# Performance work log

Measured on AMD Instinct MI355X. Metric: run time of the kernel, lower is better.

The kernel has to match this reference:

```python
import jax, jax.numpy as jnp
import numpy as np

EPSILON = 0.1
MAX_ITER = 100
THRESHOLD = 0.001
NORMALIZE = True
INPUT_SCALE = 0.02  # keeps exp(-cost/eps) from underflowing with randn inputs


def setup_inputs() -> dict:
    key = jax.random.key(0)
    k1, k2 = jax.random.split(key)
    compressed_tokens = jax.random.normal(k1, (16, 64, 768), dtype=jnp.float32) * INPUT_SCALE
    original_tokens = jax.random.normal(k2, (16, 1024, 768), dtype=jnp.float32) * INPUT_SCALE
    return {"compressed_tokens": compressed_tokens, "original_tokens": original_tokens}


def _cost_matrix(source, target):
    # pairwise squared Euclidean distances: (n, m)
    source_sq = jnp.sum(source ** 2, axis=1, keepdims=True)          # (n, 1)
    target_sq = jnp.sum(target ** 2, axis=1, keepdims=True)          # (m, 1)
    cross = source @ target.T                                         # (n, m)
    return source_sq + target_sq.T - 2.0 * cross


def _sinkhorn(K, a, b):
    n, m = K.shape
    u0 = jnp.ones((n,), K.dtype)
    v0 = jnp.ones((m,), K.dtype)

    def step(carry, _):
        u, v, done = carry
        u_new = a / (K @ v + 1e-10)
        v_new = b / (K.T @ u_new + 1e-10)
        err = jnp.max(jnp.abs(u_new - u))
        # torch breaks AFTER the update, so the converged u,v are post-update;
        # once done, freeze u,v (equivalent to breaking out of the loop)
        u_next = jnp.where(done, u, u_new)
        v_next = jnp.where(done, v, v_new)
        done_next = done | (err < THRESHOLD)
        return (u_next, v_next, done_next), None

    (u, v, _), _ = jax.lax.scan(step, (u0, v0, jnp.asarray(False)), None, length=MAX_ITER)
    return u, v


def reference(compressed_tokens, original_tokens):
    d = compressed_tokens.shape[-1]
    src = compressed_tokens.reshape(-1, d)   # (n, d)
    tgt = original_tokens.reshape(-1, d)     # (m, d)
    n, m = src.shape[0], tgt.shape[0]

    cost = _cost_matrix(src, tgt)            # (n, m)
    K = jnp.exp(-cost / EPSILON)
    a = jnp.full((n,), 1.0 / n, dtype=cost.dtype)
    b = jnp.full((m,), 1.0 / m, dtype=cost.dtype)

    u, v = _sinkhorn(K, a, b)

    # <P, C> with P = diag(u) K diag(v)
    ot_distance = jnp.sum((u[:, None] * K * v[None, :]) * cost)
    if NORMALIZE:
        ot_distance = ot_distance / (n + m)
    ot_loss = jnp.sqrt(ot_distance + 1e-8)
    return ot_loss
```

## Files before the change

kernel.cpp:

```cpp
#include <hip/hip_runtime.h>

#define NSRC 1024
#define MTGT 16384
#define DDIM 768
#define MAXIT 100
#define NBLK 256
#define NTHR 1024
#define NGRP 16
#define GRPSZ 16

typedef __attribute__((ext_vector_type(8))) short bf16x8;
typedef __attribute__((ext_vector_type(4))) float f32x4;
typedef __attribute__((ext_vector_type(4))) unsigned short u16x4;
typedef __attribute__((ext_vector_type(8))) unsigned short u16x8;

__device__ __forceinline__ unsigned short f2bf(float f) {
  unsigned u = __float_as_uint(f);
  u += 0x7FFFu + ((u >> 16) & 1u);
  return (unsigned short)(u >> 16);
}
__device__ __forceinline__ float bf2f(unsigned short h) {
  return __uint_as_float(((unsigned)h) << 16);
}
__device__ __forceinline__ void gstoref(float* p, float x) {
  __hip_atomic_store(p, x, __ATOMIC_RELAXED, __HIP_MEMORY_SCOPE_AGENT);
}
__device__ __forceinline__ float gloadf(const float* p) {
  return __hip_atomic_load(p, __ATOMIC_RELAXED, __HIP_MEMORY_SCOPE_AGENT);
}
__device__ __forceinline__ unsigned gloadu(const unsigned* p) {
  return __hip_atomic_load(p, __ATOMIC_RELAXED, __HIP_MEMORY_SCOPE_AGENT);
}
__device__ __forceinline__ void gl_lds16(const unsigned short* g, unsigned short* l) {
  __builtin_amdgcn_global_load_lds((__attribute__((address_space(1))) void*)g,
                                   (__attribute__((address_space(3))) void*)l, 16, 0, 0);
}

__global__ __launch_bounds__(192) void ot_convert_kernel(
    const float* __restrict__ src, const float* __restrict__ tgt,
    unsigned short* __restrict__ srcb, unsigned short* __restrict__ tgtb,
    float* __restrict__ ssq, float* __restrict__ tsq, unsigned* __restrict__ zreg) {
  __shared__ float sbuf[3];
  const int row = blockIdx.x;
  const float* inp;
  unsigned short* outp;
  if (row < NSRC) { inp = src + (size_t)row * DDIM; outp = srcb + (size_t)row * DDIM; }
  else { inp = tgt + (size_t)(row - NSRC) * DDIM; outp = tgtb + (size_t)(row - NSRC) * DDIM; }
  float4 v = *(const float4*)(inp + threadIdx.x * 4);
  u16x4 b; b[0] = f2bf(v.x); b[1] = f2bf(v.y); b[2] = f2bf(v.z); b[3] = f2bf(v.w);
  *(u16x4*)(outp + threadIdx.x * 4) = b;
  float acc = v.x * v.x + v.y * v.y + v.z * v.z + v.w * v.w;
  #pragma unroll
  for (int off = 32; off > 0; off >>= 1) acc += __shfl_down(acc, off, 64);
  int wave = threadIdx.x >> 6, lane = threadIdx.x & 63;
  if (lane == 0) sbuf[wave] = acc;
  __syncthreads();
  if (threadIdx.x == 0) {
    float t = sbuf[0] + sbuf[1] + sbuf[2];
    if (row < NSRC) ssq[row] = t; else tsq[row - NSRC] = t;
  }
  if (row < 576) zreg[row * 192 + threadIdx.x] = 0u;
}

__global__ __launch_bounds__(256) void ot_gemmk_kernel(
    const unsigned short* __restrict__ srcb, const unsigned short* __restrict__ tgtb,
    const float* __restrict__ ssq, const float* __restrict__ tsq,
    unsigned short* __restrict__ Kb, float* __restrict__ rowsum) {
  __shared__ __align__(16) unsigned short As[128 * 64];
  __shared__ __align__(16) unsigned short Bs[128 * 64];
  const int tile = (blockIdx.x & 7) * 128 + (blockIdx.x >> 3);
  const int tm = tile & 7, tn = tile >> 3;
  const int row0 = tm * 128, col0 = tn * 128;
  const int tid = threadIdx.x, lane = tid & 63, wave = tid >> 6;
  const int wm = wave >> 1, wn = wave & 1;
  const int lr = lane & 15, hi = lane >> 4;

  f32x4 acc[4][4];
  #pragma unroll
  for (int fi = 0; fi < 4; ++fi)
    #pragma unroll
    for (int fj = 0; fj < 4; ++fj) acc[fi][fj] = (f32x4){0.f, 0.f, 0.f, 0.f};

  for (int kt = 0; kt < DDIM / 64; ++kt) {
    __syncthreads();
    #pragma unroll
    for (int q = 0; q < 4; ++q) {
      int ch = tid + q * 256;
      int r = ch >> 3, c = ch & 7;
      int cg = c ^ (r & 7);
      gl_lds16(srcb + (size_t)(row0 + r) * DDIM + kt * 64 + cg * 8, As + ch * 8);
      gl_lds16(tgtb + (size_t)(col0 + r) * DDIM + kt * 64 + cg * 8, Bs + ch * 8);
    }
    __syncthreads();
    #pragma unroll
    for (int kc = 0; kc < 2; ++kc) {
      bf16x8 a[4], b[4];
      #pragma unroll
      for (int f = 0; f < 4; ++f) {
        int ra = wm * 64 + f * 16 + lr;
        a[f] = *(const bf16x8*)(As + ra * 64 + ((((kc << 2) | hi) ^ (ra & 7)) << 3));
        int rb = wn * 64 + f * 16 + lr;
        b[f] = *(const bf16x8*)(Bs + rb * 64 + ((((kc << 2) | hi) ^ (rb & 7)) << 3));
      }
      #pragma unroll
      for (int fi = 0; fi < 4; ++fi)
        #pragma unroll
        for (int fj = 0; fj < 4; ++fj)
          acc[fi][fj] = __builtin_amdgcn_mfma_f32_16x16x32_bf16(a[fi], b[fj], acc[fi][fj], 0, 0, 0);
    }
  }

  const float SC = 14.426950408889634f;
  int colv[4]; float tqv[4];
  #pragma unroll
  for (int fj = 0; fj < 4; ++fj) {
    colv[fj] = col0 + wn * 64 + fj * 16 + lr;
    tqv[fj] = tsq[colv[fj]];
  }
  #pragma unroll
  for (int fi = 0; fi < 4; ++fi) {
    #pragma unroll
    for (int e = 0; e < 4; ++e) {
      int row = row0 + wm * 64 + fi * 16 + hi * 4 + e;
      float sq = ssq[row];
      float p = 0.f;
      #pragma unroll
      for (int fj = 0; fj < 4; ++fj) {
        float cost = sq + tqv[fj] - 2.0f * acc[fi][fj][e];
        float k = exp2f(-SC * cost);
        Kb[(size_t)row * MTGT + colv[fj]] = f2bf(k);
        p += k;
      }
      p += __shfl_xor(p, 1, 64);
      p += __shfl_xor(p, 2, 64);
      p += __shfl_xor(p, 4, 64);
      p += __shfl_xor(p, 8, 64);
      if (lr == 0) atomicAdd(&rowsum[row], p);
    }
  }
}

__device__ __forceinline__ void grid_barrier(unsigned* garr, unsigned* root,
                                             unsigned* gen, unsigned& t) {
  __syncthreads();
  if (threadIdx.x == 0) {
    asm volatile("s_waitcnt vmcnt(0)" ::: "memory");
    unsigned g = (unsigned)(blockIdx.x >> 4);
    unsigned old = __hip_atomic_fetch_add(&garr[g * 64], 1u, __ATOMIC_RELAXED,
                                          __HIP_MEMORY_SCOPE_AGENT);
    if (old == t * GRPSZ + (GRPSZ - 1)) {
      unsigned r = __hip_atomic_fetch_add(root, 1u, __ATOMIC_RELAXED,
                                          __HIP_MEMORY_SCOPE_AGENT);
      if (r == t * NGRP + (NGRP - 1)) {
        __hip_atomic_store(gen, t + 1u, __ATOMIC_RELAXED, __HIP_MEMORY_SCOPE_AGENT);
      } else {
        while (gloadu(gen) < t + 1u) __builtin_amdgcn_s_sleep(1);
      }
    } else {
      while (gloadu(gen) < t + 1u) __builtin_amdgcn_s_sleep(1);
    }
    t += 1u;
  }
  __syncthreads();
}

__global__ __launch_bounds__(NTHR) void ot_sinkhorn_kernel(
    const unsigned short* __restrict__ Kb, const float* __restrict__ rowsum,
    float* Kv, float* ot, float* __restrict__ out,
    unsigned* garr, unsigned* root, unsigned* gen) {
  __shared__ float ulds[NSRC];
  __shared__ float vlds[64];
  __shared__ float red[2048];
  __shared__ int sflag[1];
  const int tid = threadIdx.x, bid = blockIdx.x;
  const int w = tid >> 6, l = tid & 63;
  const int r8 = l >> 3, c8 = l & 7;
  const size_t colbase = (size_t)bid * 64 + c8 * 8;
  unsigned bt = 0;
  const float A_VAL = 1.0f / NSRC, B_VAL = 1.0f / MTGT;
  float uold = 1.0f;

  for (int it = 0; it < MAXIT; ++it) {
    float kv;
    if (it == 0) {
      kv = rowsum[tid];
    } else {
      float4 va = *(const float4*)(&vlds[c8 * 8]);
      float4 vb = *(const float4*)(&vlds[c8 * 8 + 4]);
      float p[8];
      #pragma unroll
      for (int t = 0; t < 8; ++t) {
        int i = t * 128 + w * 8 + r8;
        u16x8 k8 = *(const u16x8*)(Kb + (size_t)i * MTGT + colbase);
        p[t] = bf2f(k8[0]) * va.x + bf2f(k8[1]) * va.y +
               bf2f(k8[2]) * va.z + bf2f(k8[3]) * va.w +
               bf2f(k8[4]) * vb.x + bf2f(k8[5]) * vb.y +
               bf2f(k8[6]) * vb.z + bf2f(k8[7]) * vb.w;
      }
      #pragma unroll
      for (int t = 0; t < 8; ++t) {
        p[t] += __shfl_xor(p[t], 1, 64);
        p[t] += __shfl_xor(p[t], 2, 64);
        p[t] += __shfl_xor(p[t], 4, 64);
      }
      float* kvs = Kv + (size_t)(it - 1) * NSRC;
      if (c8 == 0) {
        #pragma unroll
        for (int t = 0; t < 8; ++t) atomicAdd(&kvs[t * 128 + w * 8 + r8], p[t]);
      }
      grid_barrier(garr, root, gen, bt);
      kv = gloadf(&kvs[tid]);
    }
    float un = A_VAL / (kv + 1e-10f);
    float d = fabsf(un - uold);
    #pragma unroll
    for (int off = 32; off > 0; off >>= 1) d = fmaxf(d, __shfl_xor(d, off, 64));
    if (l == 0) red[w] = d;
    ulds[tid] = un;
    uold = un;
    __syncthreads();
    if (tid == 0) {
      float dm = red[0];
      #pragma unroll
      for (int k = 1; k < 16; ++k) dm = fmaxf(dm, red[k]);
      sflag[0] = (dm < 0.001f) ? 1 : 0;
    }
    __syncthreads();
    const bool last = (sflag[0] != 0) || (it == MAXIT - 1);

    float acc8[8], w8[8];
    #pragma unroll
    for (int e = 0; e < 8; ++e) { acc8[e] = 0.f; w8[e] = 0.f; }
    #pragma unroll
    for (int t = 0; t < 8; ++t) {
      int i = t * 128 + w * 8 + r8;
      float ui = ulds[i];
      u16x8 k8 = *(const u16x8*)(Kb + (size_t)i * MTGT + colbase);
      #pragma unroll
      for (int e = 0; e < 8; ++e) {
        float k = bf2f(k8[e]);
        acc8[e] += k * ui;
        if (last) w8[e] += (k > 0.f) ? ui * k * (-0.1f * __logf(k)) : 0.f;
      }
    }
    #pragma unroll
    for (int e = 0; e < 8; ++e) {
      acc8[e] += __shfl_xor(acc8[e], 8, 64);
      acc8[e] += __shfl_xor(acc8[e], 16, 64);
      acc8[e] += __shfl_xor(acc8[e], 32, 64);
      if (last) {
        w8[e] += __shfl_xor(w8[e], 8, 64);
        w8[e] += __shfl_xor(w8[e], 16, 64);
        w8[e] += __shfl_xor(w8[e], 32, 64);
      }
    }
    if (r8 == 0) {
      #pragma unroll
      for (int e = 0; e < 8; ++e) {
        red[w * 64 + c8 * 8 + e] = acc8[e];
        red[1024 + w * 64 + c8 * 8 + e] = w8[e];
      }
    }
    __syncthreads();
    if (tid < 64) {
      float t = 0.f, ww = 0.f;
      #pragma unroll
      for (int k16 = 0; k16 < 16; ++k16) {
        t += red[k16 * 64 + tid];
        if (last) ww += red[1024 + k16 * 64 + tid];
      }
      float vj = B_VAL / (t + 1e-10f);
      vlds[tid] = vj;
      if (last) {
        float term = ww * vj;
        #pragma unroll
        for (int off = 32; off > 0; off >>= 1) term += __shfl_down(term, off, 64);
        if (tid == 0) atomicAdd(ot, term);
      }
    }
    __syncthreads();
    if (last) break;
  }

  grid_barrier(garr, root, gen, bt);
  if (bid == 0 && tid == 0)
    out[0] = sqrtf(gloadf(ot) / (float)(NSRC + MTGT) + 1e-8f);
}

extern "C" void kernel_launch(void* const* d_in, const int* in_sizes, int n_in,
                              void* d_out, int out_size, void* d_ws, size_t ws_size,
                              hipStream_t stream) {
  const float* src = (const float*)d_in[0];
  const float* tgt = (const float*)d_in[1];
  float* out = (float*)d_out;
  char* ws = (char*)d_ws;

  unsigned short* Kb = (unsigned short*)ws;
  char* ctrl = ws + 33554432;
  float* rowsum = (float*)(ctrl);
  float* ot = (float*)(ctrl + 4608);
  unsigned* garr = (unsigned*)(ctrl + 4864);
  unsigned* root = (unsigned*)(ctrl + 8960);
  unsigned* gen  = (unsigned*)(ctrl + 9216);
  float* Kv = (float*)(ws + 33570816);
  unsigned short* srcb = (unsigned short*)(ws + 33996800);
  unsigned short* tgtb = (unsigned short*)(ws + 35569664);
  float* ssq  = (float*)(ws + 60735488);
  float* tsq  = (float*)(ws + 60739584);

  ot_convert_kernel<<<NSRC + MTGT, 192, 0, stream>>>(src, tgt, srcb, tgtb, ssq, tsq,
                                                     (unsigned*)ctrl);
  ot_gemmk_kernel<<<(NSRC / 128) * (MTGT / 128), 256, 0, stream>>>(srcb, tgtb, ssq, tsq,
                                                                   Kb, rowsum);
  ot_sinkhorn_kernel<<<NBLK, NTHR, 0, stream>>>(Kb, rowsum, Kv, ot, out, garr, root, gen);
}
```

Baseline: 189.9 us.

## Fuse cost GEMM into persistent Sinkhorn kernel with K resident in LDS

The cost GEMM and exp step now run inside the persistent Sinkhorn kernel. Each block computes its 1024x64 slice of K and keeps it in LDS as bf16 (128KB), instead of writing a 32MB K to global memory and rereading it every iteration. Target rows are converted to bf16 on the fly, with double buffering, and the source conversion moves into a small prep kernel. This removes per-iteration HBM traffic on K and one kernel launch. In exchange it uses a very large LDS footprint, computes the GEMM with only 256 blocks, and adds a grid barrier at iteration zero.

```diff
diff --git a/kernel.cpp b/kernel.cpp
--- a/kernel.cpp
+++ b/kernel.cpp
@@ -22,122 +22,38 @@
 __device__ __forceinline__ float bf2f(unsigned short h) {
   return __uint_as_float(((unsigned)h) << 16);
 }
-__device__ __forceinline__ void gstoref(float* p, float x) {
-  __hip_atomic_store(p, x, __ATOMIC_RELAXED, __HIP_MEMORY_SCOPE_AGENT);
-}
 __device__ __forceinline__ float gloadf(const float* p) {
   return __hip_atomic_load(p, __ATOMIC_RELAXED, __HIP_MEMORY_SCOPE_AGENT);
 }
 __device__ __forceinline__ unsigned gloadu(const unsigned* p) {
   return __hip_atomic_load(p, __ATOMIC_RELAXED, __HIP_MEMORY_SCOPE_AGENT);
 }
-__device__ __forceinline__ void gl_lds16(const unsigned short* g, unsigned short* l) {
-  __builtin_amdgcn_global_load_lds((__attribute__((address_space(1))) void*)g,
-                                   (__attribute__((address_space(3))) void*)l, 16, 0, 0);
-}
-
-__global__ __launch_bounds__(192) void ot_convert_kernel(
-    const float* __restrict__ src, const float* __restrict__ tgt,
-    unsigned short* __restrict__ srcb, unsigned short* __restrict__ tgtb,
-    float* __restrict__ ssq, float* __restrict__ tsq, unsigned* __restrict__ zreg) {
-  __shared__ float sbuf[3];
-  const int row = blockIdx.x;
-  const float* inp;
-  unsigned short* outp;
-  if (row < NSRC) { inp = src + (size_t)row * DDIM; outp = srcb + (size_t)row * DDIM; }
-  else { inp = tgt + (size_t)(row - NSRC) * DDIM; outp = tgtb + (size_t)(row - NSRC) * DDIM; }
-  float4 v = *(const float4*)(inp + threadIdx.x * 4);
-  u16x4 b; b[0] = f2bf(v.x); b[1] = f2bf(v.y); b[2] = f2bf(v.z); b[3] = f2bf(v.w);
-  *(u16x4*)(outp + threadIdx.x * 4) = b;
-  float acc = v.x * v.x + v.y * v.y + v.z * v.z + v.w * v.w;
+
+__global__ __launch_bounds__(256) void ot_prep_kernel(
+    const float* __restrict__ src, unsigned short* __restrict__ Ab,
+    float* __restrict__ ssq, float* __restrict__ Kv, unsigned* __restrict__ ctrl) {
+  const int gid = blockIdx.x * 256 + threadIdx.x;
   #pragma unroll
-  for (int off = 32; off > 0; off >>= 1) acc += __shfl_down(acc, off, 64);
-  int wave = threadIdx.x >> 6, lane = threadIdx.x & 63;
-  if (lane == 0) sbuf[wave] = acc;
-  __syncthreads();
-  if (threadIdx.x == 0) {
-    float t = sbuf[0] + sbuf[1] + sbuf[2];
-    if (row < NSRC) ssq[row] = t; else tsq[row - NSRC] = t;
-  }
-  if (row < 576) zreg[row * 192 + threadIdx.x] = 0u;
-}
-
-__global__ __launch_bounds__(256) void ot_gemmk_kernel(
-    const unsigned short* __restrict__ srcb, const unsigned short* __restrict__ tgtb,
-    const float* __restrict__ ssq, const float* __restrict__ tsq,
-    unsigned short* __restrict__ Kb, float* __restrict__ rowsum) {
-  __shared__ __align__(16) unsigned short As[128 * 64];
-  __shared__ __align__(16) unsigned short Bs[128 * 64];
-  const int tile = (blockIdx.x & 7) * 128 + (blockIdx.x >> 3);
-  const int tm = tile & 7, tn = tile >> 3;
-  const int row0 = tm * 128, col0 = tn * 128;
-  const int tid = threadIdx.x, lane = tid & 63, wave = tid >> 6;
-  const int wm = wave >> 1, wn = wave & 1;
-  const int lr = lane & 15, hi = lane >> 4;
-
-  f32x4 acc[4][4];
-  #pragma unroll
-  for (int fi = 0; fi < 4; ++fi)
-    #pragma unroll
-    for (int fj = 0; fj < 4; ++fj) acc[fi][fj] = (f32x4){0.f, 0.f, 0.f, 0.f};
-
-  for (int kt = 0; kt < DDIM / 64; ++kt) {
-    __syncthreads();
-    #pragma unroll
-    for (int q = 0; q < 4; ++q) {
-      int ch = tid + q * 256;
-      int r = ch >> 3, c = ch & 7;
-      int cg = c ^ (r & 7);
-      gl_lds16(srcb + (size_t)(row0 + r) * DDIM + kt * 64 + cg * 8, As + ch * 8);
-      gl_lds16(tgtb + (size_t)(col0 + r) * DDIM + kt * 64 + cg * 8, Bs + ch * 8);
-    }
-    __syncthreads();
-    #pragma unroll
-    for (int kc = 0; kc < 2; ++kc) {
-      bf16x8 a[4], b[4];
-      #pragma unroll
-      for (int f = 0; f < 4; ++f) {
-        int ra = wm * 64 + f * 16 + lr;
-        a[f] = *(const bf16x8*)(As + ra * 64 + ((((kc << 2) | hi) ^ (ra & 7)) << 3));
-        int rb = wn * 64 + f * 16 + lr;
-        b[f] = *(const bf16x8*)(Bs + rb * 64 + ((((kc << 2) | hi) ^ (rb & 7)) << 3));
-      }
-      #pragma unroll
-      for (int fi = 0; fi < 4; ++fi)
-        #pragma unroll
-        for (int fj = 0; fj < 4; ++fj)
-          acc[fi][fj] = __builtin_amdgcn_mfma_f32_16x16x32_bf16(a[fi], b[fj], acc[fi][fj], 0, 0, 0);
-    }
-  }
-
-  const float SC = 14.426950408889634f;
-  int colv[4]; float tqv[4];
-  #pragma unroll
-  for (int fj = 0; fj < 4; ++fj) {
-    colv[fj] = col0 + wn * 64 + fj * 16 + lr;
-    tqv[fj] = tsq[colv[fj]];
-  }
-  #pragma unroll
-  for (int fi = 0; fi < 4; ++fi) {
-    #pragma unroll
-    for (int e = 0; e < 4; ++e) {
-      int row = row0 + wm * 64 + fi * 16 + hi * 4 + e;
-      float sq = ssq[row];
-      float p = 0.f;
-      #pragma unroll
-      for (int fj = 0; fj < 4; ++fj) {
-        float cost = sq + tqv[fj] - 2.0f * acc[fi][fj][e];
-        float k = exp2f(-SC * cost);
-        Kb[(size_t)row * MTGT + colv[fj]] = f2bf(k);
-        p += k;
-      }
-      p += __shfl_xor(p, 1, 64);
-      p += __shfl_xor(p, 2, 64);
-      p += __shfl_xor(p, 4, 64);
-      p += __shfl_xor(p, 8, 64);
-      if (lr == 0) atomicAdd(&rowsum[row], p);
-    }
-  }
+  for (int k = 0; k < 3; ++k) {
+    int idx = gid + k * 65536;
+    float4 a = *(const float4*)(src + (size_t)idx * 4);
+    u16x4 b; b[0] = f2bf(a.x); b[1] = f2bf(a.y); b[2] = f2bf(a.z); b[3] = f2bf(a.w);
+    *(u16x4*)(Ab + (size_t)idx * 4) = b;
+  }
+  {
+    int row = gid >> 6, l = gid & 63;
+    float s = 0.f;
+    #pragma unroll
+    for (int k = 0; k < 3; ++k) {
+      float4 a = *(const float4*)(src + (size_t)row * DDIM + (l + k * 64) * 4);
+      s += a.x * a.x + a.y * a.y + a.z * a.z + a.w * a.w;
+    }
+    #pragma unroll
+    for (int off = 32; off > 0; off >>= 1) s += __shfl_down(s, off, 64);
+    if (l == 0) ssq[row] = s;
+  }
+  for (int i = gid; i < MAXIT * NSRC; i += 65536) Kv[i] = 0.f;
+  if (gid < 4096) ctrl[gid] = 0u;
 }
 
 __device__ __forceinline__ void grid_barrier(unsigned* garr, unsigned* root,
@@ -164,118 +80,170 @@
   __syncthreads();
 }
 
-__global__ __launch_bounds__(NTHR) void ot_sinkhorn_kernel(
-    const unsigned short* __restrict__ Kb, const float* __restrict__ rowsum,
+__global__ __launch_bounds__(NTHR) void ot_fused_kernel(
+    const float* __restrict__ tgt, const unsigned short* __restrict__ Ab,
+    const float* __restrict__ ssq,
     float* Kv, float* ot, float* __restrict__ out,
     unsigned* garr, unsigned* root, unsigned* gen) {
+  __shared__ __align__(16) unsigned short Ks[NSRC * 64];
+  __shared__ __align__(16) unsigned short Bs[2][4096];
   __shared__ float ulds[NSRC];
+  __shared__ float red[1104];
   __shared__ float vlds[64];
-  __shared__ float red[2048];
-  __shared__ int sflag[1];
+  __shared__ float tsql[64];
+  __shared__ int sflag;
+
   const int tid = threadIdx.x, bid = blockIdx.x;
   const int w = tid >> 6, l = tid & 63;
-  const int r8 = l >> 3, c8 = l & 7;
-  const size_t colbase = (size_t)bid * 64 + c8 * 8;
+  const int lr = l & 15, hi = l >> 4;
+  const int m0 = w * 64;
+  const size_t c0 = (size_t)bid * 64;
+  const int rB = tid >> 4, kq = tid & 15;
   unsigned bt = 0;
   const float A_VAL = 1.0f / NSRC, B_VAL = 1.0f / MTGT;
+
+  f32x4 acc[4][4];
+  #pragma unroll
+  for (int fi = 0; fi < 4; ++fi)
+    #pragma unroll
+    for (int fj = 0; fj < 4; ++fj) acc[fi][fj] = (f32x4){0.f, 0.f, 0.f, 0.f};
+
+  float tsq_part = 0.f;
+  {
+    float4 bv = *(const float4*)(tgt + (c0 + rB) * DDIM + kq * 4);
+    tsq_part += bv.x * bv.x + bv.y * bv.y + bv.z * bv.z + bv.w * bv.w;
+    u16x4 bb; bb[0] = f2bf(bv.x); bb[1] = f2bf(bv.y); bb[2] = f2bf(bv.z); bb[3] = f2bf(bv.w);
+    *(u16x4*)(&Bs[0][rB * 64 + (((kq >> 1) ^ (rB & 7)) << 3) + ((kq & 1) << 2)]) = bb;
+  }
+  __syncthreads();
+
+  for (int kt = 0; kt < 12; ++kt) {
+    float4 bv;
+    if (kt < 11)
+      bv = *(const float4*)(tgt + (c0 + rB) * DDIM + (kt + 1) * 64 + kq * 4);
+    #pragma unroll
+    for (int kc = 0; kc < 2; ++kc) {
+      bf16x8 a[4];
+      #pragma unroll
+      for (int fi = 0; fi < 4; ++fi)
+        a[fi] = *(const bf16x8*)(Ab + (size_t)(m0 + fi * 16 + lr) * DDIM +
+                                 kt * 64 + kc * 32 + hi * 8);
+      #pragma unroll
+      for (int fj = 0; fj < 4; ++fj) {
+        int rb = fj * 16 + lr;
+        bf16x8 b = *(const bf16x8*)(&Bs[kt & 1][rb * 64 + ((((kc << 2) | hi) ^ (rb & 7)) << 3)]);
+        #pragma unroll
+        for (int fi = 0; fi < 4; ++fi)
+          acc[fi][fj] = __builtin_amdgcn_mfma_f32_16x16x32_bf16(a[fi], b, acc[fi][fj], 0, 0, 0);
+      }
+    }
+    if (kt < 11) {
+      tsq_part += bv.x * bv.x + bv.y * bv.y + bv.z * bv.z + bv.w * bv.w;
+      u16x4 bb; bb[0] = f2bf(bv.x); bb[1] = f2bf(bv.y); bb[2] = f2bf(bv.z); bb[3] = f2bf(bv.w);
+      *(u16x4*)(&Bs[(kt + 1) & 1][rB * 64 + (((kq >> 1) ^ (rB & 7)) << 3) + ((kq & 1) << 2)]) = bb;
+    }
+    __syncthreads();
+  }
+
+  {
+    float s = tsq_part;
+    s += __shfl_xor(s, 1, 64); s += __shfl_xor(s, 2, 64);
+    s += __shfl_xor(s, 4, 64); s += __shfl_xor(s, 8, 64);
+    if (kq == 0) tsql[rB] = s;
+  }
+  __syncthreads();
+
+  {
+    const float SC = 14.426950408889634f;
+    #pragma unroll
+    for (int fi = 0; fi < 4; ++fi) {
+      #pragma unroll
+      for (int e = 0; e < 4; ++e) {
+        int r = m0 + fi * 16 + hi * 4 + e;
+        float sq = ssq[r];
+        #pragma unroll
+        for (int fj = 0; fj < 4; ++fj) {
+          int c = fj * 16 + lr;
+          float cost = sq + tsql[c] - 2.0f * acc[fi][fj][e];
+          float k = exp2f(-SC * cost);
+          Ks[r * 64 + (((c >> 3) ^ (r & 7)) << 3) + (c & 7)] = f2bf(k);
+        }
+      }
+    }
+  }
+  if (tid < 64) vlds[tid] = 1.0f;
+  __syncthreads();
+
   float uold = 1.0f;
-
   for (int it = 0; it < MAXIT; ++it) {
-    float kv;
-    if (it == 0) {
-      kv = rowsum[tid];
-    } else {
-      float4 va = *(const float4*)(&vlds[c8 * 8]);
-      float4 vb = *(const float4*)(&vlds[c8 * 8 + 4]);
-      float p[8];
-      #pragma unroll
-      for (int t = 0; t < 8; ++t) {
-        int i = t * 128 + w * 8 + r8;
-        u16x8 k8 = *(const u16x8*)(Kb + (size_t)i * MTGT + colbase);
-        p[t] = bf2f(k8[0]) * va.x + bf2f(k8[1]) * va.y +
-               bf2f(k8[2]) * va.z + bf2f(k8[3]) * va.w +
-               bf2f(k8[4]) * vb.x + bf2f(k8[5]) * vb.y +
-               bf2f(k8[6]) * vb.z + bf2f(k8[7]) * vb.w;
-      }
-      #pragma unroll
-      for (int t = 0; t < 8; ++t) {
-        p[t] += __shfl_xor(p[t], 1, 64);
-        p[t] += __shfl_xor(p[t], 2, 64);
-        p[t] += __shfl_xor(p[t], 4, 64);
-      }
-      float* kvs = Kv + (size_t)(it - 1) * NSRC;
-      if (c8 == 0) {
-        #pragma unroll
-        for (int t = 0; t < 8; ++t) atomicAdd(&kvs[t * 128 + w * 8 + r8], p[t]);
-      }
-      grid_barrier(garr, root, gen, bt);
-      kv = gloadf(&kvs[tid]);
-    }
-    float un = A_VAL / (kv + 1e-10f);
-    float d = fabsf(un - uold);
-    #pragma unroll
-    for (int off = 32; off > 0; off >>= 1) d = fmaxf(d, __shfl_xor(d, off, 64));
-    if (l == 0) red[w] = d;
-    ulds[tid] = un;
-    uold = un;
+    {
+      const int i = tid;
+      float p = 0.f;
+      #pragma unroll
+      for (int lu = 0; lu < 8; ++lu) {
+        int su = lu ^ (i & 7);
+        u16x8 k8 = *(const u16x8*)(&Ks[i * 64 + su * 8]);
+        float4 va = *(const float4*)(&vlds[lu * 8]);
+        float4 vb = *(const float4*)(&vlds[lu * 8 + 4]);
+        p += bf2f(k8[0]) * va.x + bf2f(k8[1]) * va.y +
+             bf2f(k8[2]) * va.z + bf2f(k8[3]) * va.w +
+             bf2f(k8[4]) * vb.x + bf2f(k8[5]) * vb.y +
+             bf2f(k8[6]) * vb.z + bf2f(k8[7]) * vb.w;
+      }
+      atomicAdd(&Kv[it * NSRC + i], p);
+    }
+    grid_barrier(garr, root, gen, bt);
+    float un, d;
+    {
+      float kv = gloadf(&Kv[it * NSRC + tid]);
+      un = A_VAL / (kv + 1e-10f);
+      d = fabsf(un - uold);
+      #pragma unroll
+      for (int off = 32; off > 0; off >>= 1) d = fmaxf(d, __shfl_xor(d, off, 64));
+      if (l == 0) red[w] = d;
+      ulds[tid] = un;
+      uold = un;
+    }
     __syncthreads();
     if (tid == 0) {
       float dm = red[0];
       #pragma unroll
       for (int k = 1; k < 16; ++k) dm = fmaxf(dm, red[k]);
-      sflag[0] = (dm < 0.001f) ? 1 : 0;
-    }
-    __syncthreads();
-    const bool last = (sflag[0] != 0) || (it == MAXIT - 1);
-
-    float acc8[8], w8[8];
-    #pragma unroll
-    for (int e = 0; e < 8; ++e) { acc8[e] = 0.f; w8[e] = 0.f; }
-    #pragma unroll
-    for (int t = 0; t < 8; ++t) {
-      int i = t * 128 + w * 8 + r8;
-      float ui = ulds[i];
-      u16x8 k8 = *(const u16x8*)(Kb + (size_t)i * MTGT + colbase);
-      #pragma unroll
-      for (int e = 0; e < 8; ++e) {
-        float k = bf2f(k8[e]);
-        acc8[e] += k * ui;
-        if (last) w8[e] += (k > 0.f) ? ui * k * (-0.1f * __logf(k)) : 0.f;
-      }
-    }
-    #pragma unroll
-    for (int e = 0; e < 8; ++e) {
-      acc8[e] += __shfl_xor(acc8[e], 8, 64);
-      acc8[e] += __shfl_xor(acc8[e], 16, 64);
-      acc8[e] += __shfl_xor(acc8[e], 32, 64);
-      if (last) {
-        w8[e] += __shfl_xor(w8[e], 8, 64);
-        w8[e] += __shfl_xor(w8[e], 16, 64);
-        w8[e] += __shfl_xor(w8[e], 32, 64);
-      }
-    }
-    if (r8 == 0) {
-      #pragma unroll
-      for (int e = 0; e < 8; ++e) {
-        red[w * 64 + c8 * 8 + e] = acc8[e];
-        red[1024 + w * 64 + c8 * 8 + e] = w8[e];
-      }
-    }
-    __syncthreads();
-    if (tid < 64) {
+      sflag = (dm < 0.001f) ? 1 : 0;
+    }
+    __syncthreads();
+    const bool last = (sflag != 0) || (it == MAXIT - 1);
+
+    {
+      float* wred = (float*)Bs;
+      const int c = l;
       float t = 0.f, ww = 0.f;
-      #pragma unroll
-      for (int k16 = 0; k16 < 16; ++k16) {
-        t += red[k16 * 64 + tid];
-        if (last) ww += red[1024 + k16 * 64 + tid];
-      }
-      float vj = B_VAL / (t + 1e-10f);
-      vlds[tid] = vj;
-      if (last) {
-        float term = ww * vj;
+      #pragma unroll 8
+      for (int r = 0; r < 64; ++r) {
+        int i = w * 64 + r;
+        float ui = ulds[i];
+        float k = bf2f(Ks[i * 64 + (((c >> 3) ^ (i & 7)) << 3) + (c & 7)]);
+        t += k * ui;
+        if (last) ww += (k > 0.f) ? ui * k * (-0.1f * __logf(k)) : 0.f;
+      }
+      red[w * 68 + c] = t;
+      if (last) wred[w * 68 + c] = ww;
+      __syncthreads();
+      if (tid < 64) {
+        float tt = 0.f, wsum = 0.f;
         #pragma unroll
-        for (int off = 32; off > 0; off >>= 1) term += __shfl_down(term, off, 64);
-        if (tid == 0) atomicAdd(ot, term);
+        for (int g = 0; g < 16; ++g) {
+          tt += red[g * 68 + tid];
+          if (last) wsum += wred[g * 68 + tid];
+        }
+        float vj = B_VAL / (tt + 1e-10f);
+        vlds[tid] = vj;
+        if (last) {
+          float term = wsum * vj;
+          #pragma unroll
+          for (int off = 32; off > 0; off >>= 1) term += __shfl_down(term, off, 64);
+          if (tid == 0) atomicAdd(ot, term);
+        }
       }
     }
     __syncthreads();
@@ -295,22 +263,16 @@
   float* out = (float*)d_out;
   char* ws = (char*)d_ws;
 
-  unsigned short* Kb = (unsigned short*)ws;
-  char* ctrl = ws + 33554432;
-  float* rowsum = (float*)(ctrl);
-  float* ot = (float*)(ctrl + 4608);
-  unsigned* garr = (unsigned*)(ctrl + 4864);
-  unsigned* root = (unsigned*)(ctrl + 8960);
-  unsigned* gen  = (unsigned*)(ctrl + 9216);
-  float* Kv = (float*)(ws + 33570816);
-  unsigned short* srcb = (unsigned short*)(ws + 33996800);
-  unsigned short* tgtb = (unsigned short*)(ws + 35569664);
-  float* ssq  = (float*)(ws + 60735488);
-  float* tsq  = (float*)(ws + 60739584);
-
-  ot_convert_kernel<<<NSRC + MTGT, 192, 0, stream>>>(src, tgt, srcb, tgtb, ssq, tsq,
-                                                     (unsigned*)ctrl);
-  ot_gemmk_kernel<<<(NSRC / 128) * (MTGT / 128), 256, 0, stream>>>(srcb, tgtb, ssq, tsq,
-                                                                   Kb, rowsum);
-  ot_sinkhorn_kernel<<<NBLK, NTHR, 0, stream>>>(Kb, rowsum, Kv, ot, out, garr, root, gen);
-}
+  unsigned short* Ab = (unsigned short*)(ws);
+  float* ssq = (float*)(ws + 1572864);
+  float* Kv  = (float*)(ws + 1576960);
+  unsigned* ctrl = (unsigned*)(ws + 1986560);
+  unsigned* garr = ctrl;
+  unsigned* root = ctrl + 1024;
+  unsigned* gen  = ctrl + 1040;
+  float* ot      = (float*)(ctrl + 1056);
+
+  ot_prep_kernel<<<256, 256, 0, stream>>>(src, Ab, ssq, Kv, ctrl);
+  ot_fused_kernel<<<NBLK, NTHR, 0, stream>>>(tgt, Ab, ssq, Kv, ot, out,
+                                             garr, root, gen);
+}
```

New measurement: 179.1 us. 5.7% less time.
